# Kernel optimization log

Measured on AMD Instinct MI355X. Metric: run time of the kernel, lower is better.

## Reference

```python
import jax, jax.numpy as jnp
import numpy as np

THRESH = 1e-6
EPS = 1e-8
LN_EPS = 1e-5


def _layer(h, M, W_in, b_in, W_out, b_out, W_self, b_self, gamma, beta):
    # Normalize incoming flows per destination column: A[j,i] = M[j,i]/sum_k M[k,i]
    A = M / (jnp.sum(M, axis=0, keepdims=True) + EPS)
    mask = A > THRESH
    W = jnp.where(mask, A, 0.0)                      # thresholded edge weights [N,N]
    T = h @ W_in + b_in                              # transformed features [N,out]
    weighted_sum = jnp.einsum('ji,jd->id', W, T)     # sum over origins j per dest i
    weight_sum = jnp.sum(W, axis=0)                  # [N]
    has_edge = jnp.any(mask, axis=0)                 # dest i has >=1 incoming edge
    agg = jnp.where(has_edge[:, None],
                    weighted_sum / (weight_sum[:, None] + EPS),
                    T)
    agg = agg @ W_out + b_out                        # dropout is identity in eval
    out = agg + (h @ W_self + b_self)                # residual (dims differ -> self_transform)
    mu = jnp.mean(out, axis=-1, keepdims=True)
    var = jnp.mean(jnp.square(out - mu), axis=-1, keepdims=True)
    out = (out - mu) * jax.lax.rsqrt(var + LN_EPS) * gamma + beta
    return out


def setup_inputs() -> dict:
    key = jax.random.key(0)
    ks = jax.random.split(key, 16)
    N, D_IN, D_H, D_OUT = 8192, 256, 512, 256
    s = 0.05
    return {
        'node_features': jax.random.normal(ks[0], (N, D_IN), jnp.float32),
        'mobility_matrix': jax.random.uniform(ks[1], (N, N), jnp.float32),
        # layer 1: in -> hidden
        'W_in1': jax.random.normal(ks[2], (D_IN, D_H)) * s,
        'b_in1': jnp.zeros((D_H,)),
        'W_out1': jax.random.normal(ks[3], (D_H, D_H)) * s,
        'b_out1': jnp.zeros((D_H,)),
        'W_self1': jax.random.normal(ks[4], (D_IN, D_H)) * s,
        'b_self1': jnp.zeros((D_H,)),
        'g1': jnp.ones((D_H,)),
        'be1': jnp.zeros((D_H,)),
        # layer 2: hidden -> out
        'W_in2': jax.random.normal(ks[5], (D_H, D_OUT)) * s,
        'b_in2': jnp.zeros((D_OUT,)),
        'W_out2': jax.random.normal(ks[6], (D_OUT, D_OUT)) * s,
        'b_out2': jnp.zeros((D_OUT,)),
        'W_self2': jax.random.normal(ks[7], (D_H, D_OUT)) * s,
        'b_self2': jnp.zeros((D_OUT,)),
        'g2': jnp.ones((D_OUT,)),
        'be2': jnp.zeros((D_OUT,)),
    }


def reference(node_features, mobility_matrix,
              W_in1, b_in1, W_out1, b_out1, W_self1, b_self1, g1, be1,
              W_in2, b_in2, W_out2, b_out2, W_self2, b_self2, g2, be2):
    h = _layer(node_features, mobility_matrix,
               W_in1, b_in1, W_out1, b_out1, W_self1, b_self1, g1, be1)
    h = jax.nn.relu(h)  # inter-layer activation
    h = _layer(h, mobility_matrix,
               W_in2, b_in2, W_out2, b_out2, W_self2, b_self2, g2, be2)
    h = jax.nn.relu(h)  # final activation
    return h
```

## Files before the change

### kernel.cpp

```cpp
#include <hip/hip_runtime.h>
#include <stdint.h>

typedef short bf16x8 __attribute__((ext_vector_type(8)));
typedef short s16x4 __attribute__((ext_vector_type(4)));
typedef float f32x4 __attribute__((ext_vector_type(4)));
typedef unsigned int u32;

#define EPS_A 1e-8f
#define THR_A 1e-6f
#define NN 8192

static __device__ __forceinline__ short f2bf(float f) {
  u32 u = __float_as_uint(f);
  u = u + 0x7FFFu + ((u >> 16) & 1u);
  return (short)(u >> 16);
}
static __device__ __forceinline__ float bf2f(short s) {
  return __uint_as_float(((u32)(unsigned short)s) << 16);
}
static __device__ __forceinline__ int swz(int row, int slot8) {
  int off = row * 32 + slot8 * 8;
  return off ^ (((row >> 1) & 7) << 3);
}
static __device__ __forceinline__ void gld16(const short* g, short* l) {
  __builtin_amdgcn_global_load_lds(
      (const __attribute__((address_space(1))) u32*)g,
      (__attribute__((address_space(3))) u32*)l, 16, 0, 0);
}

__global__ __launch_bounds__(256) void k_prep_mt(
    const float* __restrict__ M, short* __restrict__ Mt,
    float* __restrict__ colsum, u32* __restrict__ colmax)
{
  __shared__ __align__(16) short tile[256 * 66];
  const int t = threadIdx.x;
  const int i0 = blockIdx.x * 256;
  const int j0 = blockIdx.y * 64;
  const int i = i0 + t;
  float s = 0.f, mx = 0.f;
  #pragma unroll 4
  for (int jj = 0; jj < 64; ++jj) {
    float v = M[(size_t)(j0 + jj) * NN + i];
    s += v;
    mx = fmaxf(mx, v);
    tile[t * 66 + jj] = f2bf(v);
  }
  atomicAdd(&colsum[i], s);
  atomicMax(&colmax[i], __float_as_uint(mx));
  __syncthreads();
  #pragma unroll
  for (int p = 0; p < 8; ++p) {
    const int r = p * 32 + (t >> 3);
    const int c = t & 7;
    const u32* src = (const u32*)((const char*)tile + r * 132 + c * 16);
    int4 w = make_int4(src[0], src[1], src[2], src[3]);
    *(int4*)((char*)Mt + (((size_t)(i0 + r) * NN + j0) * 2 + c * 16)) = w;
  }
}

__global__ __launch_bounds__(256) void k_prep_fused(
    const float* __restrict__ nf,
    const float* __restrict__ W_in1, const float* __restrict__ W_out1,
    const float* __restrict__ W_self1, const float* __restrict__ W_in2,
    const float* __restrict__ W_out2, const float* __restrict__ W_self2,
    const float* __restrict__ b_in1, const float* __restrict__ b_out1,
    const float* __restrict__ b_self1, const float* __restrict__ b_out2,
    const float* __restrict__ b_self2,
    short* __restrict__ nft, short* __restrict__ A1cat, short* __restrict__ Win1b,
    short* __restrict__ Wout1t, short* __restrict__ Bcat1, short* __restrict__ Win2t,
    short* __restrict__ Bcat2, float* __restrict__ bias1c, float* __restrict__ bias2c)
{
  int b = blockIdx.x;
  const int t = threadIdx.x;
  if (b < 512) {
    __shared__ short tile[64][65];
    const int r0 = (b & 127) * 64, c0 = (b >> 7) * 64;
    #pragma unroll
    for (int p = 0; p < 16; ++p) {
      const int rr = p * 4 + (t >> 6), cc = t & 63;
      tile[rr][cc] = f2bf(nf[(size_t)(r0 + rr) * 256 + c0 + cc]);
    }
    __syncthreads();
    #pragma unroll
    for (int q = 0; q < 16; ++q) {
      const int cc = q * 4 + (t >> 6), rr = t & 63;
      nft[(size_t)(c0 + cc) * 8192 + r0 + rr] = tile[rr][cc];
    }
    return;
  }
  b -= 512;
  if (b < 2048) {
    const int idx = b * 256 + t;
    const float4 v = ((const float4*)nf)[idx];
    const int i = idx >> 6;
    const int c = (idx & 63) * 4;
    s16x4 o;
    o.x = f2bf(v.x); o.y = f2bf(v.y); o.z = f2bf(v.z); o.w = f2bf(v.w);
    *(s16x4*)&A1cat[(size_t)i * 512 + 256 + c] = o;
    return;
  }
  b -= 2048;
  if (b < 128) {
    const int idx = b * 256 + t;
    const float4 v = ((const float4*)W_in1)[idx];
    s16x4 o;
    o.x = f2bf(v.x); o.y = f2bf(v.y); o.z = f2bf(v.z); o.w = f2bf(v.w);
    *(s16x4*)&Win1b[idx * 4] = o;
    return;
  }
  b -= 128;
  if (b < 1024) {
    const int idx = b * 256 + t;
    const int r = idx >> 9, c = idx & 511;
    Wout1t[(size_t)c * 512 + r] = f2bf(W_out1[idx]);
    return;
  }
  b -= 1024;
  if (b < 512) {
    const int idx = b * 256 + t;
    const int r = idx >> 9, c = idx & 511;
    Bcat1[(size_t)c * 512 + 256 + r] = f2bf(W_self1[idx]);
    return;
  }
  b -= 512;
  if (b < 512) {
    const int idx = b * 256 + t;
    const int r = idx >> 8, c = idx & 255;
    Win2t[(size_t)c * 512 + r] = f2bf(W_in2[idx]);
    return;
  }
  b -= 512;
  if (b < 256) {
    const int idx = b * 256 + t;
    const int r = idx >> 8, c = idx & 255;
    Bcat2[(size_t)c * 768 + r] = f2bf(W_out2[idx]);
    return;
  }
  b -= 256;
  if (b < 512) {
    const int idx = b * 256 + t;
    const int r = idx >> 8, c = idx & 255;
    Bcat2[(size_t)c * 768 + 256 + r] = f2bf(W_self2[idx]);
    return;
  }
  b -= 512;
  if (b < 2) {
    const int n = b * 256 + t;
    float a = b_out1[n] + b_self1[n];
    for (int p = 0; p < 512; ++p) a += b_in1[p] * W_out1[(size_t)p * 512 + n];
    bias1c[n] = a;
    return;
  }
  bias2c[t] = b_out2[t] + b_self2[t];
}

template <int BN, int EPI>
__device__ __forceinline__ void gemm_body(
    const short* __restrict__ A, const short* __restrict__ B, int K, int ldA, int ldB,
    void* __restrict__ Cout, int ldC, const float* __restrict__ bias0)
{
  constexpr int BM = 64;
  constexpr int MI = BM / 32;
  constexpr int NI = BN / 32;
  constexpr int LDP = 40;
  __shared__ __align__(16) short As[BM * LDP];
  __shared__ __align__(16) short Bs[BN * LDP];
  const int t = threadIdx.x;

  const int gx = gridDim.x;
  int flat = blockIdx.y * gx + blockIdx.x;
  const int cpx = (gx * gridDim.y) >> 3;
  flat = (flat & 7) * cpx + (flat >> 3);
  const int bx = flat % gx, by = flat / gx;
  const int m0 = by * BM, n0 = bx * BN;

  const int wid = t >> 6, l = t & 63;
  const int wr = wid >> 1, wc = wid & 1;
  const int lr = l & 15, lk = l >> 4;

  f32x4 acc[MI][NI] = {};

  const int sr = t >> 2;
  const int sc = (t & 3) * 8;
  const short* gA0 = A + (size_t)(m0 + sr) * ldA + sc;
  const short* gB0 = B + (size_t)(n0 + sr) * ldB + sc;
  const short* gB1 = gB0 + (size_t)64 * ldB;

  for (int k0 = 0; k0 < K; k0 += 32) {
    const int4 a0 = *(const int4*)(gA0 + k0);
    const int4 b0 = *(const int4*)(gB0 + k0);
    int4 b1 = make_int4(0, 0, 0, 0);
    if (NI == 4) b1 = *(const int4*)(gB1 + k0);
    __syncthreads();
    *(int4*)&As[sr * LDP + sc] = a0;
    *(int4*)&Bs[sr * LDP + sc] = b0;
    if (NI == 4) *(int4*)&Bs[(64 + sr) * LDP + sc] = b1;
    __syncthreads();

    bf16x8 av[MI], bv[NI];
    #pragma unroll
    for (int mi = 0; mi < MI; ++mi)
      av[mi] = *(const bf16x8*)&As[(wr * (BM / 2) + mi * 16 + lr) * LDP + lk * 8];
    #pragma unroll
    for (int ni = 0; ni < NI; ++ni)
      bv[ni] = *(const bf16x8*)&Bs[(wc * (BN / 2) + ni * 16 + lr) * LDP + lk * 8];
    #pragma unroll
    for (int mi = 0; mi < MI; ++mi)
      #pragma unroll
      for (int ni = 0; ni < NI; ++ni)
        acc[mi][ni] = __builtin_amdgcn_mfma_f32_16x16x32_bf16(av[mi], bv[ni], acc[mi][ni], 0, 0, 0);
  }

  #pragma unroll
  for (int mi = 0; mi < MI; ++mi) {
    #pragma unroll
    for (int r = 0; r < 4; ++r) {
      const int m = m0 + wr * (BM / 2) + mi * 16 + lk * 4 + r;
      float b0 = 0.f;
      if (EPI == 0) b0 = bias0[m];
      #pragma unroll
      for (int ni = 0; ni < NI; ++ni) {
        const int n = n0 + wc * (BN / 2) + ni * 16 + lr;
        float v = acc[mi][ni][r];
        if (EPI == 0) {
          v += b0;
          ((short*)Cout)[(size_t)m * ldC + n] = f2bf(v);
        } else if (EPI == 3) {
          ((short*)Cout)[(size_t)m * ldC + n] = f2bf(v);
        } else {
          v += bias0[n];
          ((float*)Cout)[(size_t)m * ldC + n] = v;
        }
      }
    }
  }
}

__global__ __launch_bounds__(256) void k_gemm_bias_n(
    const short* __restrict__ A, const short* __restrict__ B, int K, int ldA, int ldB,
    void* __restrict__ C, int ldC, const float* __restrict__ bias0) {
  gemm_body<64, 0>(A, B, K, ldA, ldB, C, ldC, bias0);
}
__global__ __launch_bounds__(256) void k_gemm_raw_n(
    const short* __restrict__ A, const short* __restrict__ B, int K, int ldA, int ldB,
    void* __restrict__ C, int ldC) {
  gemm_body<64, 3>(A, B, K, ldA, ldB, C, ldC, nullptr);
}
__global__ __launch_bounds__(256) void k_gemm_out_w(
    const short* __restrict__ A, const short* __restrict__ B, int K, int ldA, int ldB,
    void* __restrict__ C, int ldC, const float* __restrict__ bias0) {
  gemm_body<128, 2>(A, B, K, ldA, ldB, C, ldC, bias0);
}
__global__ __launch_bounds__(256) void k_gemm_out_n(
    const short* __restrict__ A, const short* __restrict__ B, int K, int ldA, int ldB,
    void* __restrict__ C, int ldC, const float* __restrict__ bias0) {
  gemm_body<64, 2>(A, B, K, ldA, ldB, C, ldC, bias0);
}

__global__ __launch_bounds__(256) void k_gemm_sk128(
    const short* __restrict__ A, const short* __restrict__ B, int K, int ldA, int ldB,
    short* __restrict__ P, int ldC, size_t pstride)
{
  __shared__ __align__(16) short As[128 * 32];
  __shared__ __align__(16) short Bs[128 * 32];
  const int t = threadIdx.x;

  const int sk = blockIdx.z;
  A += (size_t)sk * K;
  B += (size_t)sk * K;

  const int gx = gridDim.x;
  int flat = blockIdx.y * gx + blockIdx.x;
  const int cpx = (gx * gridDim.y) >> 3;
  flat = (flat & 7) * cpx + (flat >> 3);
  const int bx = flat % gx, by = flat / gx;
  const int m0 = by * 128, n0 = bx * 128;

  const int wid = t >> 6, l = t & 63;
  const int wr = wid >> 1, wc = wid & 1;
  const int lr = l & 15, lk = l >> 4;

  f32x4 acc[4][4] = {};

  const int side = wid >> 1;
  const int hu = (wid & 1) * 256;
  const short* Xp = side ? B : A;
  const int ldX = side ? ldB : ldA;
  const int x0 = side ? n0 : m0;
  short* dbase = (side ? Bs : As) + hu * 8;
  const short *g0, *g1, *g2, *g3;
  {
    int u, off, msk, orig, row, slot;
    u = hu + 0 * 64 + l; off = u * 8; msk = ((off >> 6) & 7) << 3; orig = off ^ msk;
    row = orig >> 5; slot = (orig >> 3) & 3;
    g0 = Xp + (size_t)(x0 + row) * ldX + slot * 8;
    u = hu + 1 * 64 + l; off = u * 8; msk = ((off >> 6) & 7) << 3; orig = off ^ msk;
    row = orig >> 5; slot = (orig >> 3) & 3;
    g1 = Xp + (size_t)(x0 + row) * ldX + slot * 8;
    u = hu + 2 * 64 + l; off = u * 8; msk = ((off >> 6) & 7) << 3; orig = off ^ msk;
    row = orig >> 5; slot = (orig >> 3) & 3;
    g2 = Xp + (size_t)(x0 + row) * ldX + slot * 8;
    u = hu + 3 * 64 + l; off = u * 8; msk = ((off >> 6) & 7) << 3; orig = off ^ msk;
    row = orig >> 5; slot = (orig >> 3) & 3;
    g3 = Xp + (size_t)(x0 + row) * ldX + slot * 8;
  }

  for (int k0 = 0; k0 < K; k0 += 32) {
    __syncthreads();
    gld16(g0 + k0, dbase);
    gld16(g1 + k0, dbase + 512);
    gld16(g2 + k0, dbase + 1024);
    gld16(g3 + k0, dbase + 1536);
    __syncthreads();

    bf16x8 av[4], bv[4];
    #pragma unroll
    for (int mi = 0; mi < 4; ++mi)
      av[mi] = *(const bf16x8*)&As[swz(wr * 64 + mi * 16 + lr, lk)];
    #pragma unroll
    for (int ni = 0; ni < 4; ++ni)
      bv[ni] = *(const bf16x8*)&Bs[swz(wc * 64 + ni * 16 + lr, lk)];
    #pragma unroll
    for (int mi = 0; mi < 4; ++mi)
      #pragma unroll
      for (int ni = 0; ni < 4; ++ni)
        acc[mi][ni] = __builtin_amdgcn_mfma_f32_16x16x32_bf16(av[mi], bv[ni], acc[mi][ni], 0, 0, 0);
  }

  short* outp = P + pstride * sk;
  #pragma unroll
  for (int mi = 0; mi < 4; ++mi) {
    #pragma unroll
    for (int r = 0; r < 4; ++r) {
      const int m = m0 + wr * 64 + mi * 16 + lk * 4 + r;
      #pragma unroll
      for (int ni = 0; ni < 4; ++ni) {
        const int n = n0 + wc * 64 + ni * 16 + lr;
        outp[(size_t)m * ldC + n] = f2bf(acc[mi][ni][r]);
      }
    }
  }
}

__global__ __launch_bounds__(256) void k_sk_reduce_sub(
    const short* __restrict__ P, int N, size_t pstride, int S,
    const float* __restrict__ colsum, const u32* __restrict__ colmax,
    const short* __restrict__ hraw, int ldh,
    short* __restrict__ out, int ldo)
{
  const int idx = blockIdx.x * 256 + threadIdx.x;
  const int nq = N >> 2;
  const int m = idx / nq;
  const int c4 = (idx - m * nq) * 4;
  const size_t base = (size_t)m * N + c4;
  float a0 = 0.f, a1 = 0.f, a2 = 0.f, a3 = 0.f;
  for (int s = 0; s < S; ++s) {
    s16x4 v = *(const s16x4*)&P[pstride * s + base];
    a0 += bf2f(v.x); a1 += bf2f(v.y); a2 += bf2f(v.z); a3 += bf2f(v.w);
  }
  const float cs = colsum[m];
  const float rc = 1.f / (cs + EPS_A);
  const float rcw = rc / (cs * rc + EPS_A);
  const bool he = __uint_as_float(colmax[m]) * rc > THR_A;
  s16x4 o;
  if (he) {
    o.x = f2bf(a0 * rcw); o.y = f2bf(a1 * rcw);
    o.z = f2bf(a2 * rcw); o.w = f2bf(a3 * rcw);
  } else {
    o = *(const s16x4*)&hraw[(size_t)m * ldh + c4];
  }
  *(s16x4*)&out[(size_t)m * ldo + c4] = o;
}

__global__ __launch_bounds__(256) void k_sk_reduce(
    const short* __restrict__ P, int N, size_t pstride, int S,
    const float* __restrict__ colsum, const u32* __restrict__ colmax,
    const short* __restrict__ Tfall, short* __restrict__ out, int ldo)
{
  const int idx = blockIdx.x * 256 + threadIdx.x;
  const int nq = N >> 2;
  const int m = idx / nq;
  const int c4 = (idx - m * nq) * 4;
  const size_t base = (size_t)m * N + c4;
  float a0 = 0.f, a1 = 0.f, a2 = 0.f, a3 = 0.f;
  for (int s = 0; s < S; ++s) {
    s16x4 v = *(const s16x4*)&P[pstride * s + base];
    a0 += bf2f(v.x); a1 += bf2f(v.y); a2 += bf2f(v.z); a3 += bf2f(v.w);
  }
  const float cs = colsum[m];
  const float rc = 1.f / (cs + EPS_A);
  const float rcw = rc / (cs * rc + EPS_A);
  const bool he = __uint_as_float(colmax[m]) * rc > THR_A;
  a0 *= rcw; a1 *= rcw; a2 *= rcw; a3 *= rcw;
  if (__ballot(!he)) {
    if (!he) {
      a0 = bf2f(Tfall[(size_t)(c4 + 0) * NN + m]);
      a1 = bf2f(Tfall[(size_t)(c4 + 1) * NN + m]);
      a2 = bf2f(Tfall[(size_t)(c4 + 2) * NN + m]);
      a3 = bf2f(Tfall[(size_t)(c4 + 3) * NN + m]);
    }
  }
  s16x4 o;
  o.x = f2bf(a0); o.y = f2bf(a1); o.z = f2bf(a2); o.w = f2bf(a3);
  *(s16x4*)&out[(size_t)m * ldo + c4] = o;
}

template <int MODE>
__device__ __forceinline__ void ln_relu_body(
    const float* __restrict__ X, int W,
    const float* __restrict__ g, const float* __restrict__ be,
    void* __restrict__ out, int ldo)
{
  const int row = blockIdx.x;
  const int t = threadIdx.x;
  const float* x = X + (size_t)row * W;
  float v0 = x[t], v1 = 0.f;
  float s = v0, ss = v0 * v0;
  if (W == 512) { v1 = x[t + 256]; s += v1; ss += v1 * v1; }
  #pragma unroll
  for (int off = 32; off; off >>= 1) {
    s += __shfl_down(s, off);
    ss += __shfl_down(ss, off);
  }
  __shared__ float red[8];
  const int wid = t >> 6;
  if ((t & 63) == 0) { red[wid] = s; red[4 + wid] = ss; }
  __syncthreads();
  s = red[0] + red[1] + red[2] + red[3];
  ss = red[4] + red[5] + red[6] + red[7];
  const float mu = s / W;
  const float var = ss / W - mu * mu;
  const float sc = rsqrtf(var + 1e-5f);
  float y = fmaxf((v0 - mu) * sc * g[t] + be[t], 0.f);
  if (MODE == 0) ((short*)out)[(size_t)row * ldo + t] = f2bf(y);
  else           ((float*)out)[(size_t)row * ldo + t] = y;
  if (W == 512) {
    float y1 = fmaxf((v1 - mu) * sc * g[t + 256] + be[t + 256], 0.f);
    if (MODE == 0) ((short*)out)[(size_t)row * ldo + t + 256] = f2bf(y1);
    else           ((float*)out)[(size_t)row * ldo + t + 256] = y1;
  }
}

__global__ __launch_bounds__(256) void k_ln_relu_bf16(
    const float* __restrict__ X, int W, const float* __restrict__ g,
    const float* __restrict__ be, short* __restrict__ out, int ldo) {
  ln_relu_body<0>(X, W, g, be, out, ldo);
}
__global__ __launch_bounds__(256) void k_ln_relu_f32(
    const float* __restrict__ X, int W, const float* __restrict__ g,
    const float* __restrict__ be, float* __restrict__ out, int ldo) {
  ln_relu_body<1>(X, W, g, be, out, ldo);
}

extern "C" void kernel_launch(void* const* d_in, const int* in_sizes, int n_in,
                              void* d_out, int out_size, void* d_ws, size_t ws_size,
                              hipStream_t stream) {
  const float* nf      = (const float*)d_in[0];
  const float* Mob     = (const float*)d_in[1];
  const float* W_in1   = (const float*)d_in[2];
  const float* b_in1   = (const float*)d_in[3];
  const float* W_out1  = (const float*)d_in[4];
  const float* b_out1  = (const float*)d_in[5];
  const float* W_self1 = (const float*)d_in[6];
  const float* b_self1 = (const float*)d_in[7];
  const float* g1      = (const float*)d_in[8];
  const float* be1     = (const float*)d_in[9];
  const float* W_in2   = (const float*)d_in[10];
  const float* b_in2   = (const float*)d_in[11];
  const float* W_out2  = (const float*)d_in[12];
  const float* b_out2  = (const float*)d_in[13];
  const float* W_self2 = (const float*)d_in[14];
  const float* b_self2 = (const float*)d_in[15];
  const float* g2      = (const float*)d_in[16];
  const float* be2     = (const float*)d_in[17];

  char* ws = (char*)d_ws;
  float* colsum = (float*)(ws);
  u32*   colmax = (u32*)(ws + 32768);
  short* Mt     = (short*)(ws + 65536);
  short* nft    = (short*)(ws + 134283264);
  short* A1cat  = (short*)(ws + 138477568);
  float* C2f    = (float*)(ws + 146866176);
  short* Acat2  = (short*)(ws + 163643392);
  short* T2t    = (short*)(ws + 176226304);
  short* Bcat1  = (short*)(ws + 180420608);
  short* Bcat2  = (short*)(ws + 180944896);
  short* Win2t  = (short*)(ws + 181338112);
  short* Wout1t = (short*)(ws + 181600256);
  short* Win1b  = (short*)(ws + 182124544);
  float* bias1c = (float*)(ws + 182386688);
  float* bias2c = (float*)(ws + 182390784);
  short* P1     = (short*)(ws + 188743680);
  short* P2     = (short*)(ws + 222298112);

  hipMemsetAsync(ws, 0, 65536, stream);

  k_prep_mt<<<dim3(32, 128), 256, 0, stream>>>(Mob, Mt, colsum, colmax);
  k_prep_fused<<<5507, 256, 0, stream>>>(nf, W_in1, W_out1, W_self1, W_in2, W_out2,
                                         W_self2, b_in1, b_out1, b_self1, b_out2,
                                         b_self2, nft, A1cat, Win1b, Wout1t, Bcat1,
                                         Win2t, Bcat2, bias1c, bias2c);
  k_gemm_raw_n<<<dim3(4, 8), 256, 0, stream>>>(Wout1t, Win1b, 512, 512, 512,
                                               Bcat1, 512);

  k_gemm_sk128<<<dim3(2, 64, 8), 256, 0, stream>>>(Mt, nft, 1024, NN, NN,
                                                   P1, 256, (size_t)8192 * 256);
  k_sk_reduce_sub<<<2048, 256, 0, stream>>>(P1, 256, (size_t)8192 * 256, 8,
                                            colsum, colmax, A1cat + 256, 512,
                                            A1cat, 512);
  k_gemm_out_w<<<dim3(4, 128), 256, 0, stream>>>(A1cat, Bcat1, 512, 512, 512,
                                                 C2f, 512, bias1c);
  k_ln_relu_bf16<<<8192, 256, 0, stream>>>(C2f, 512, g1, be1, Acat2 + 256, 768);

  k_gemm_bias_n<<<dim3(128, 4), 256, 0, stream>>>(Win2t, Acat2 + 256, 512, 512, 768,
                                                  T2t, NN, b_in2);
  k_gemm_sk128<<<dim3(2, 64, 8), 256, 0, stream>>>(Mt, T2t, 1024, NN, NN,
                                                   P2, 256, (size_t)8192 * 256);
  k_sk_reduce<<<2048, 256, 0, stream>>>(P2, 256, (size_t)8192 * 256, 8,
                                        colsum, colmax, T2t, Acat2, 768);
  k_gemm_out_n<<<dim3(4, 128), 256, 0, stream>>>(Acat2, Bcat2, 768, 768, 768,
                                                 C2f, 256, bias2c);
  k_ln_relu_f32<<<8192, 256, 0, stream>>>(C2f, 256, g2, be2, (float*)d_out, 256);
}
```

Measured before the change: 325.0 us.

## Merge prep kernels and deepen split-K GEMM to 64-wide K tiles with staggered start

Folds the mobility-matrix transpose/colsum kernel into the fused prep kernel so one launch covers all prep blocks and they can overlap. The split-K GEMM now loads 64-wide K slices per iteration with a simpler XOR swizzle, halving the barrier count per K, and starts each block at a rotated K offset to spread memory traffic across blocks. This doubles LDS per block, which may lower occupancy, and the shared buffer size now applies to every prep block.

```diff
diff --git a/kernel.cpp b/kernel.cpp
--- a/kernel.cpp
+++ b/kernel.cpp
@@ -18,62 +18,56 @@
 static __device__ __forceinline__ float bf2f(short s) {
   return __uint_as_float(((u32)(unsigned short)s) << 16);
 }
-static __device__ __forceinline__ int swz(int row, int slot8) {
-  int off = row * 32 + slot8 * 8;
-  return off ^ (((row >> 1) & 7) << 3);
-}
 static __device__ __forceinline__ void gld16(const short* g, short* l) {
   __builtin_amdgcn_global_load_lds(
       (const __attribute__((address_space(1))) u32*)g,
       (__attribute__((address_space(3))) u32*)l, 16, 0, 0);
 }
 
-__global__ __launch_bounds__(256) void k_prep_mt(
-    const float* __restrict__ M, short* __restrict__ Mt,
-    float* __restrict__ colsum, u32* __restrict__ colmax)
-{
-  __shared__ __align__(16) short tile[256 * 66];
-  const int t = threadIdx.x;
-  const int i0 = blockIdx.x * 256;
-  const int j0 = blockIdx.y * 64;
-  const int i = i0 + t;
-  float s = 0.f, mx = 0.f;
-  #pragma unroll 4
-  for (int jj = 0; jj < 64; ++jj) {
-    float v = M[(size_t)(j0 + jj) * NN + i];
-    s += v;
-    mx = fmaxf(mx, v);
-    tile[t * 66 + jj] = f2bf(v);
-  }
-  atomicAdd(&colsum[i], s);
-  atomicMax(&colmax[i], __float_as_uint(mx));
-  __syncthreads();
-  #pragma unroll
-  for (int p = 0; p < 8; ++p) {
-    const int r = p * 32 + (t >> 3);
-    const int c = t & 7;
-    const u32* src = (const u32*)((const char*)tile + r * 132 + c * 16);
-    int4 w = make_int4(src[0], src[1], src[2], src[3]);
-    *(int4*)((char*)Mt + (((size_t)(i0 + r) * NN + j0) * 2 + c * 16)) = w;
-  }
-}
-
-__global__ __launch_bounds__(256) void k_prep_fused(
-    const float* __restrict__ nf,
+__global__ __launch_bounds__(256) void k_prep_all(
+    const float* __restrict__ Mob, const float* __restrict__ nf,
     const float* __restrict__ W_in1, const float* __restrict__ W_out1,
     const float* __restrict__ W_self1, const float* __restrict__ W_in2,
     const float* __restrict__ W_out2, const float* __restrict__ W_self2,
     const float* __restrict__ b_in1, const float* __restrict__ b_out1,
     const float* __restrict__ b_self1, const float* __restrict__ b_out2,
     const float* __restrict__ b_self2,
+    short* __restrict__ Mt, float* __restrict__ colsum, u32* __restrict__ colmax,
     short* __restrict__ nft, short* __restrict__ A1cat, short* __restrict__ Win1b,
     short* __restrict__ Wout1t, short* __restrict__ Bcat1, short* __restrict__ Win2t,
     short* __restrict__ Bcat2, float* __restrict__ bias1c, float* __restrict__ bias2c)
 {
+  __shared__ __align__(16) short sbuf[256 * 66];
   int b = blockIdx.x;
   const int t = threadIdx.x;
+  if (b < 4096) {
+    const int i0 = (b & 31) * 256;
+    const int j0 = (b >> 5) * 64;
+    const int i = i0 + t;
+    float s = 0.f, mx = 0.f;
+    #pragma unroll 4
+    for (int jj = 0; jj < 64; ++jj) {
+      float v = Mob[(size_t)(j0 + jj) * NN + i];
+      s += v;
+      mx = fmaxf(mx, v);
+      sbuf[t * 66 + jj] = f2bf(v);
+    }
+    atomicAdd(&colsum[i], s);
+    atomicMax(&colmax[i], __float_as_uint(mx));
+    __syncthreads();
+    #pragma unroll
+    for (int p = 0; p < 8; ++p) {
+      const int r = p * 32 + (t >> 3);
+      const int c = t & 7;
+      const u32* src = (const u32*)((const char*)sbuf + r * 132 + c * 16);
+      int4 w = make_int4(src[0], src[1], src[2], src[3]);
+      *(int4*)((char*)Mt + (((size_t)(i0 + r) * NN + j0) * 2 + c * 16)) = w;
+    }
+    return;
+  }
+  b -= 4096;
   if (b < 512) {
-    __shared__ short tile[64][65];
+    short (*tile)[65] = (short(*)[65])sbuf;
     const int r0 = (b & 127) * 64, c0 = (b >> 7) * 64;
     #pragma unroll
     for (int p = 0; p < 16; ++p) {
@@ -261,8 +255,8 @@
     const short* __restrict__ A, const short* __restrict__ B, int K, int ldA, int ldB,
     short* __restrict__ P, int ldC, size_t pstride)
 {
-  __shared__ __align__(16) short As[128 * 32];
-  __shared__ __align__(16) short Bs[128 * 32];
+  __shared__ __align__(16) short As[128 * 64];
+  __shared__ __align__(16) short Bs[128 * 64];
   const int t = threadIdx.x;
 
   const int sk = blockIdx.z;
@@ -283,48 +277,51 @@
   f32x4 acc[4][4] = {};
 
   const int side = wid >> 1;
-  const int hu = (wid & 1) * 256;
+  const int hrow = (wid & 1) * 64;
   const short* Xp = side ? B : A;
   const int ldX = side ? ldB : ldA;
   const int x0 = side ? n0 : m0;
-  short* dbase = (side ? Bs : As) + hu * 8;
-  const short *g0, *g1, *g2, *g3;
-  {
-    int u, off, msk, orig, row, slot;
-    u = hu + 0 * 64 + l; off = u * 8; msk = ((off >> 6) & 7) << 3; orig = off ^ msk;
-    row = orig >> 5; slot = (orig >> 3) & 3;
-    g0 = Xp + (size_t)(x0 + row) * ldX + slot * 8;
-    u = hu + 1 * 64 + l; off = u * 8; msk = ((off >> 6) & 7) << 3; orig = off ^ msk;
-    row = orig >> 5; slot = (orig >> 3) & 3;
-    g1 = Xp + (size_t)(x0 + row) * ldX + slot * 8;
-    u = hu + 2 * 64 + l; off = u * 8; msk = ((off >> 6) & 7) << 3; orig = off ^ msk;
-    row = orig >> 5; slot = (orig >> 3) & 3;
-    g2 = Xp + (size_t)(x0 + row) * ldX + slot * 8;
-    u = hu + 3 * 64 + l; off = u * 8; msk = ((off >> 6) & 7) << 3; orig = off ^ msk;
-    row = orig >> 5; slot = (orig >> 3) & 3;
-    g3 = Xp + (size_t)(x0 + row) * ldX + slot * 8;
-  }
-
-  for (int k0 = 0; k0 < K; k0 += 32) {
+  short* dbase = (side ? Bs : As) + hrow * 64;
+  const int lrow = l >> 3, lcol = l & 7;
+  const short* g0 = Xp + (size_t)(x0 + hrow + lrow) * ldX + (lcol ^ lrow) * 8;
+  const size_t st8 = (size_t)8 * ldX;
+
+  const int niters = K >> 6;
+  int kk = (flat + sk * 3) & (niters - 1);
+
+  for (int it = 0; it < niters; ++it) {
+    const int koff = kk << 6;
+    kk = (kk + 1) & (niters - 1);
     __syncthreads();
-    gld16(g0 + k0, dbase);
-    gld16(g1 + k0, dbase + 512);
-    gld16(g2 + k0, dbase + 1024);
-    gld16(g3 + k0, dbase + 1536);
+    gld16(g0 + koff,            dbase);
+    gld16(g0 + koff + st8,      dbase + 512);
+    gld16(g0 + koff + 2 * st8,  dbase + 1024);
+    gld16(g0 + koff + 3 * st8,  dbase + 1536);
+    gld16(g0 + koff + 4 * st8,  dbase + 2048);
+    gld16(g0 + koff + 5 * st8,  dbase + 2560);
+    gld16(g0 + koff + 6 * st8,  dbase + 3072);
+    gld16(g0 + koff + 7 * st8,  dbase + 3584);
     __syncthreads();
 
-    bf16x8 av[4], bv[4];
-    #pragma unroll
-    for (int mi = 0; mi < 4; ++mi)
-      av[mi] = *(const bf16x8*)&As[swz(wr * 64 + mi * 16 + lr, lk)];
-    #pragma unroll
-    for (int ni = 0; ni < 4; ++ni)
-      bv[ni] = *(const bf16x8*)&Bs[swz(wc * 64 + ni * 16 + lr, lk)];
-    #pragma unroll
-    for (int mi = 0; mi < 4; ++mi)
+    #pragma unroll
+    for (int ks = 0; ks < 2; ++ks) {
+      bf16x8 av[4], bv[4];
       #pragma unroll
-      for (int ni = 0; ni < 4; ++ni)
-        acc[mi][ni] = __builtin_amdgcn_mfma_f32_16x16x32_bf16(av[mi], bv[ni], acc[mi][ni], 0, 0, 0);
+      for (int mi = 0; mi < 4; ++mi) {
+        const int row = wr * 64 + mi * 16 + lr;
+        av[mi] = *(const bf16x8*)&As[row * 64 + ((ks * 4 + lk) ^ (lr & 7)) * 8];
+      }
+      #pragma unroll
+      for (int ni = 0; ni < 4; ++ni) {
+        const int row = wc * 64 + ni * 16 + lr;
+        bv[ni] = *(const bf16x8*)&Bs[row * 64 + ((ks * 4 + lk) ^ (lr & 7)) * 8];
+      }
+      #pragma unroll
+      for (int mi = 0; mi < 4; ++mi)
+        #pragma unroll
+        for (int ni = 0; ni < 4; ++ni)
+          acc[mi][ni] = __builtin_amdgcn_mfma_f32_16x16x32_bf16(av[mi], bv[ni], acc[mi][ni], 0, 0, 0);
+    }
   }
 
   short* outp = P + pstride * sk;
@@ -495,11 +492,11 @@
 
   hipMemsetAsync(ws, 0, 65536, stream);
 
-  k_prep_mt<<<dim3(32, 128), 256, 0, stream>>>(Mob, Mt, colsum, colmax);
-  k_prep_fused<<<5507, 256, 0, stream>>>(nf, W_in1, W_out1, W_self1, W_in2, W_out2,
-                                         W_self2, b_in1, b_out1, b_self1, b_out2,
-                                         b_self2, nft, A1cat, Win1b, Wout1t, Bcat1,
-                                         Win2t, Bcat2, bias1c, bias2c);
+  k_prep_all<<<9603, 256, 0, stream>>>(Mob, nf, W_in1, W_out1, W_self1, W_in2,
+                                       W_out2, W_self2, b_in1, b_out1, b_self1,
+                                       b_out2, b_self2, Mt, colsum, colmax, nft,
+                                       A1cat, Win1b, Wout1t, Bcat1, Win2t, Bcat2,
+                                       bias1c, bias2c);
   k_gemm_raw_n<<<dim3(4, 8), 256, 0, stream>>>(Wout1t, Win1b, 512, 512, 512,
                                                Bcat1, 512);
 
```

Measured after the change: 312.3 us. 1.04x faster.
